# Kernel tuning notes

Hardware: AMD Instinct MI355X
Metric: run time of the kernel (lower is better)

The kernel has to match this reference:

```python
import jax, jax.numpy as jnp
import numpy as np

L = 4          # decoder layers (model_config "[4,[0],0]")
D = 1024       # d_model
H = 16         # n_head
DH = 64        # d_head
DI = 4096      # d_inner
V = 16000      # n_token (add_eot=False)
S = 1024       # seq len
B = 4          # batch
EPS = 1e-5


def _layer_norm(x, g, b):
    mu = jnp.mean(x, axis=-1, keepdims=True)
    var = jnp.mean(jnp.square(x - mu), axis=-1, keepdims=True)
    return (x - mu) * jax.lax.rsqrt(var + EPS) * g + b


def _rel_shift(x):
    # x: [b, n, q, k]
    b, n, q, k = x.shape
    zero_pad = jnp.zeros((b, n, q, 1), dtype=x.dtype)
    xp = jnp.concatenate([zero_pad, x], axis=3)        # [b,n,q,k+1]
    xp = xp.reshape(b, n, k + 1, q)
    return xp[:, :, 1:, :].reshape(b, n, q, k)


def setup_inputs() -> dict:
    key = jax.random.key(0)
    ks = list(jax.random.split(key, 24))
    sd = 0.02
    inp = {}
    inp["tokens"] = jax.random.randint(ks[0], (S, B), 0, V)
    inp["word_emb"] = jax.random.normal(ks[1], (V, D), jnp.float32) * sd
    inp["r_w_bias"] = jax.random.normal(ks[2], (H, DH), jnp.float32) * sd
    inp["r_r_bias"] = jax.random.normal(ks[3], (H, DH), jnp.float32) * sd
    inp["qkv_w"] = jax.random.normal(ks[4], (L, D, 3 * H * DH), jnp.float32) * sd
    inp["qkv_b"] = jnp.zeros((L, 3 * H * DH), jnp.float32)
    inp["r_kw"] = jax.random.normal(ks[5], (L, D, H * DH), jnp.float32) * sd
    inp["r_kb"] = jnp.zeros((L, H * DH), jnp.float32)
    inp["o_w"] = jax.random.normal(ks[6], (L, H * DH, D), jnp.float32) * sd
    inp["o_b"] = jnp.zeros((L, D), jnp.float32)
    inp["ln1_g"] = jnp.ones((L, D), jnp.float32)
    inp["ln1_b"] = jnp.zeros((L, D), jnp.float32)
    inp["ff1_w"] = jax.random.normal(ks[7], (L, D, DI), jnp.float32) * sd
    inp["ff1_b"] = jnp.zeros((L, DI), jnp.float32)
    inp["ff2_w"] = jax.random.normal(ks[8], (L, DI, D), jnp.float32) * sd
    inp["ff2_b"] = jnp.zeros((L, D), jnp.float32)
    inp["ln2_g"] = jnp.ones((L, D), jnp.float32)
    inp["ln2_b"] = jnp.zeros((L, D), jnp.float32)
    inp["final_w"] = jax.random.normal(ks[9], (D, V), jnp.float32) * sd
    inp["final_b"] = jnp.zeros((V,), jnp.float32)
    return inp


def reference(tokens, word_emb, r_w_bias, r_r_bias, qkv_w, qkv_b, r_kw, r_kb,
              o_w, o_b, ln1_g, ln1_b, ff1_w, ff1_b, ff2_w, ff2_b,
              ln2_g, ln2_b, final_w, final_b):
    s, b = tokens.shape
    h = word_emb[tokens]                                 # [S,B,D]
    # sinusoidal relative positions, pos_seq = klen-1 ... 0
    pos_seq = jnp.arange(s - 1, -1, -1, dtype=h.dtype)
    inv_freq = 1.0 / (10000.0 ** (jnp.arange(0, D, 2, dtype=h.dtype) / D))
    sinu = pos_seq[:, None] * inv_freq[None, :]
    r = jnp.concatenate([jnp.sin(sinu), jnp.cos(sinu)], axis=-1)   # [S,D]
    # causal mask: True = masked (j > i)
    mask = jnp.triu(jnp.ones((s, s), dtype=bool), k=1)
    scale = 1.0 / (DH ** 0.5)
    neg_inf = jnp.asarray(-jnp.inf, dtype=h.dtype)

    for l in range(L):
        qkv = h @ qkv_w[l] + qkv_b[l]                    # [S,B,3*H*DH]
        q, k, v = jnp.split(qkv, 3, axis=-1)
        q = q.reshape(s, b, H, DH)
        k = k.reshape(s, b, H, DH)
        v = v.reshape(s, b, H, DH)
        rk = (r @ r_kw[l] + r_kb[l]).reshape(s, H, DH)   # [S,H,DH]
        AC = jnp.einsum('ibnd,jbnd->bnij', q + r_w_bias, k)
        BD = jnp.einsum('ibnd,jnd->bnij', q + r_r_bias, rk)
        BD = _rel_shift(BD)
        score = scale * (AC + BD)
        score = jnp.where(mask[None, None, :, :], neg_inf, score)
        prob = jax.nn.softmax(score, axis=-1)
        vec = jnp.einsum('bnij,jbnd->ibnd', prob, v).reshape(s, b, H * DH)
        attn_out = vec @ o_w[l] + o_b[l]
        h = _layer_norm(h + attn_out, ln1_g[l], ln1_b[l])
        ff = jax.nn.gelu(h @ ff1_w[l] + ff1_b[l], approximate=False) @ ff2_w[l] + ff2_b[l]
        h = _layer_norm(h + ff, ln2_g[l], ln2_b[l])

    logits = h @ final_w + final_b                       # [S,B,V]
    return logits
```

## Files before the change

kernel.cpp:

```cpp
#include <hip/hip_runtime.h>

#define S 1024
#define Bb 4
#define Hh 16
#define DHh 64
#define Dm 1024
#define DIi 4096
#define Vv 16000
#define Lll 4

typedef __attribute__((ext_vector_type(4))) float f32x4;
typedef __attribute__((ext_vector_type(8))) __bf16 bf16x8;
typedef __attribute__((ext_vector_type(8))) unsigned short u16x8;
typedef __attribute__((ext_vector_type(4))) unsigned short u16x4;

__device__ __forceinline__ unsigned short f2bf(float f) {
  unsigned int u = __float_as_uint(f);
  u += 0x7fffu + ((u >> 16) & 1u);
  return (unsigned short)(u >> 16);
}
__device__ __forceinline__ float bf2f(unsigned short u) {
  return __uint_as_float(((unsigned int)u) << 16);
}

__device__ __forceinline__ void gload_lds16(const void* g, void* l) {
  __builtin_amdgcn_global_load_lds((const __attribute__((address_space(1))) unsigned int*)g,
                                   (__attribute__((address_space(3))) unsigned int*)l, 16, 0, 0);
}

__device__ __forceinline__ f32x4 mfma_bf16(bf16x8 a, bf16x8 b, f32x4 c) {
  return __builtin_amdgcn_mfma_f32_16x16x32_bf16(a, b, c, 0, 0, 0);
}

__global__ __launch_bounds__(256) void embed_k(const int* __restrict__ tokens,
                                               const float* __restrict__ we,
                                               float* __restrict__ h,
                                               unsigned short* __restrict__ hb) {
  int row = blockIdx.x;
  int t = threadIdx.x;
  int tok = tokens[row];
  f32x4 v = *(const f32x4*)&we[(long)tok * Dm + t * 4];
  *(f32x4*)&h[(long)row * Dm + t * 4] = v;
  u16x4 r;
#pragma unroll
  for (int e = 0; e < 4; ++e) r[e] = f2bf(v[e]);
  *(u16x4*)&hb[(long)row * Dm + t * 4] = r;
}

__global__ __launch_bounds__(256) void posr_k(unsigned short* __restrict__ r) {
  int idx = blockIdx.x * 256 + threadIdx.x;
  int u = idx >> 10, d = idx & 1023;
  float pos = (float)(S - 1 - u);
  int j = d & 511;
  float invf = powf(10000.0f, -(float)j * (1.0f / 512.0f));
  float a = pos * invf;
  r[idx] = f2bf(d < 512 ? sinf(a) : cosf(a));
}

__global__ __launch_bounds__(256) void wcvt_t(const float* __restrict__ W,
                                              unsigned short* __restrict__ WT,
                                              int Kd, int Nd) {
  __shared__ unsigned short tile[32][40];
  int n0 = blockIdx.x * 32, k0 = blockIdx.y * 32;
  const bool inb = n0 < Nd;
  const float* Wb = W + (long)blockIdx.z * Kd * Nd;
  unsigned short* WTb = WT + (long)blockIdx.z * Kd * Nd;
  int t = threadIdx.x;
  int rr = t >> 3, c4 = (t & 7) * 4;
  f32x4 v = {0.f, 0.f, 0.f, 0.f};
  if (inb) v = *(const f32x4*)&Wb[(long)(k0 + rr) * Nd + n0 + c4];
#pragma unroll
  for (int e = 0; e < 4; ++e) tile[rr][c4 + e] = f2bf(v[e]);
  __syncthreads();
  if (t < 128) {
    int n = t >> 2, k8 = (t & 3) * 8;
    u16x8 pk;
#pragma unroll
    for (int e = 0; e < 8; ++e) pk[e] = tile[k8 + e][n];
    *(u16x8*)&WTb[(long)(n0 + n) * Kd + k0 + k8] = pk;
  }
}

template <int EPI>
__global__ __launch_bounds__(512, 2) void gemm256(const unsigned short* __restrict__ A,
                                                  const unsigned short* __restrict__ BT,
                                                  const float* __restrict__ bias,
                                                  void* __restrict__ Cout,
                                                  int M, int N, int K,
                                                  int ntm, int ntn, int morder) {
  __shared__ unsigned short lds[65536];
  unsigned short* Al = lds;
  unsigned short* Bl = lds + 32768;
  const int tid = threadIdx.x, lane = tid & 63, w = tid >> 6;
  const int la = lane & 15, hi = lane >> 4;
  const int nwg = gridDim.x;
  const int qq = nwg >> 3, rr = nwg & 7;
  const int xcd = blockIdx.x & 7, loc = blockIdx.x >> 3;
  const int wg = (xcd < rr ? xcd * (qq + 1) : rr * (qq + 1) + (xcd - rr) * qq) + loc;
  int bm, bn;
  if (morder) { bm = (wg % ntm) * 256; bn = (wg / ntm) * 256; }
  else        { bn = (wg % ntn) * 256; bm = (wg / ntn) * 256; }
  const int wr = w >> 2, wc = w & 3;
  f32x4 acc[8][4] = {};

  const unsigned short* ag = A + (long)(bm + w * 16 + la) * K + hi * 8;
  const unsigned short* bg = BT + (long)(bn + w * 16 + la) * K + hi * 8;
  unsigned short* Asg = Al + w * 512;
  unsigned short* Bsg = Bl + w * 512;
  const unsigned short* Ard = Al + wr * 4096 + lane * 8;
  const unsigned short* Brd = Bl + wc * 2048 + lane * 8;
  const int NT = K >> 5;

#define STAGE(t) { \
    long ko_ = (long)(t) * 32; int bo_ = ((t) & 3) * 8192; \
    gload_lds16(ag + ko_, Asg + bo_); \
    gload_lds16(ag + ko_ + (long)128 * K, Asg + bo_ + 4096); \
    gload_lds16(bg + ko_, Bsg + bo_); \
    gload_lds16(bg + ko_ + (long)128 * K, Bsg + bo_ + 4096); }

#define COMPUTE(t) { \
    const int bo_ = ((t) & 3) * 8192; \
    bf16x8 af[8], bq[4]; \
    _Pragma("unroll") \
    for (int m = 0; m < 8; ++m) af[m] = *(const bf16x8*)(Ard + bo_ + m * 512); \
    _Pragma("unroll") \
    for (int n = 0; n < 4; ++n) bq[n] = *(const bf16x8*)(Brd + bo_ + n * 512); \
    __builtin_amdgcn_s_setprio(1); \
    _Pragma("unroll") \
    for (int m = 0; m < 8; ++m) \
      _Pragma("unroll") \
      for (int n = 0; n < 4; ++n) acc[m][n] = mfma_bf16(af[m], bq[n], acc[m][n]); \
    __builtin_amdgcn_s_setprio(0); }

  STAGE(0); STAGE(1); STAGE(2);
  int t = 0;
  for (; t < NT - 3; ++t) {
    asm volatile("s_waitcnt vmcnt(8)" ::: "memory");
    __builtin_amdgcn_s_barrier();
    __builtin_amdgcn_sched_barrier(0);
    STAGE(t + 3);
    COMPUTE(t);
  }
  asm volatile("s_waitcnt vmcnt(8)" ::: "memory");
  __builtin_amdgcn_s_barrier();
  __builtin_amdgcn_sched_barrier(0);
  COMPUTE(t); ++t;
  asm volatile("s_waitcnt vmcnt(4)" ::: "memory");
  __builtin_amdgcn_s_barrier();
  __builtin_amdgcn_sched_barrier(0);
  COMPUTE(t); ++t;
  asm volatile("s_waitcnt vmcnt(0)" ::: "memory");
  __builtin_amdgcn_s_barrier();
  __builtin_amdgcn_sched_barrier(0);
  COMPUTE(t);
#undef STAGE
#undef COMPUTE

#pragma unroll
  for (int m = 0; m < 8; ++m) {
#pragma unroll
    for (int n = 0; n < 4; ++n) {
      int col = bn + wc * 64 + n * 16 + la;
      if (col < N) {
        float bv = bias[col];
        int row = bm + wr * 128 + m * 16 + hi * 4;
#pragma unroll
        for (int e = 0; e < 4; ++e) {
          float v = acc[m][n][e] + bv;
          if (EPI == 0) {
            ((float*)Cout)[(long)(row + e) * N + col] = v;
          } else if (EPI == 1) {
            ((unsigned short*)Cout)[(long)(row + e) * N + col] = f2bf(v);
          } else {
            float g = 0.5f * v * (1.0f + erff(v * 0.70710678118f));
            ((unsigned short*)Cout)[(long)(row + e) * N + col] = f2bf(g);
          }
        }
      }
    }
  }
}

template <int EPI>
__global__ __launch_bounds__(256) void gemm_bt(const unsigned short* __restrict__ A,
                                               const unsigned short* __restrict__ BT,
                                               const float* __restrict__ bias,
                                               void* __restrict__ Cout,
                                               int M, int N, int K, int ntn) {
  __shared__ unsigned short As[128 * 64];
  __shared__ unsigned short Bs[128 * 64];
  const int tid = threadIdx.x;
  const int lane = tid & 63;
  const int w = tid >> 6;
  const int nwg = gridDim.x;
  const int qq = nwg >> 3, rr = nwg & 7;
  const int xcd = blockIdx.x & 7, loc = blockIdx.x >> 3;
  const int wg = (xcd < rr ? xcd * (qq + 1) : rr * (qq + 1) + (xcd - rr) * qq) + loc;
  const int bn = (wg % ntn) * 128, bm = (wg / ntn) * 128;
  const int wr = (w >> 1) * 64, wc = (w & 1) * 64;
  const int la = lane & 15, hi = lane >> 4;
  f32x4 acc[4][4] = {};

  const int rrow = tid >> 3;
  const int rcol = ((tid & 7) ^ (rrow & 7)) * 8;
  const unsigned short* ag = A + (long)(bm + rrow) * K + rcol;
  const unsigned short* bg = BT + (long)(bn + rrow) * K + rcol;
  const int las = la & 7;
  const int ro0 = (hi ^ las) * 8;
  const int ro1 = ((hi + 4) ^ las) * 8;

  for (int k0 = 0; k0 < K; k0 += 64) {
    __syncthreads();
#pragma unroll
    for (int c = 0; c < 4; ++c) {
      gload_lds16(ag + (long)c * 32 * K + k0, &As[c * 2048 + w * 512]);
      gload_lds16(bg + (long)c * 32 * K + k0, &Bs[c * 2048 + w * 512]);
    }
    __syncthreads();
#pragma unroll
    for (int kk = 0; kk < 2; ++kk) {
      const int ro = kk ? ro1 : ro0;
      bf16x8 af[4], bq[4];
#pragma unroll
      for (int mi = 0; mi < 4; ++mi)
        af[mi] = *(const bf16x8*)&As[(wr + mi * 16 + la) * 64 + ro];
#pragma unroll
      for (int ni = 0; ni < 4; ++ni)
        bq[ni] = *(const bf16x8*)&Bs[(wc + ni * 16 + la) * 64 + ro];
#pragma unroll
      for (int mi = 0; mi < 4; ++mi)
#pragma unroll
        for (int ni = 0; ni < 4; ++ni)
          acc[mi][ni] = mfma_bf16(af[mi], bq[ni], acc[mi][ni]);
    }
  }
  const int cr = hi * 4;
#pragma unroll
  for (int mi = 0; mi < 4; ++mi) {
#pragma unroll
    for (int ni = 0; ni < 4; ++ni) {
      int col = bn + wc + ni * 16 + la;
      float bv = bias[col];
      int row = bm + wr + mi * 16 + cr;
#pragma unroll
      for (int e = 0; e < 4; ++e) {
        float v = acc[mi][ni][e] + bv;
        if (EPI == 0) {
          ((float*)Cout)[(long)(row + e) * N + col] = v;
        } else if (EPI == 1) {
          ((unsigned short*)Cout)[(long)(row + e) * N + col] = f2bf(v);
        } else {
          float g = 0.5f * v * (1.0f + erff(v * 0.70710678118f));
          ((unsigned short*)Cout)[(long)(row + e) * N + col] = f2bf(g);
        }
      }
    }
  }
}

template <int EPI>
__global__ __launch_bounds__(256) void gemm_bt64(const unsigned short* __restrict__ A,
                                                 const unsigned short* __restrict__ BT,
                                                 const float* __restrict__ bias,
                                                 void* __restrict__ Cout,
                                                 int M, int N, int K, int ntn) {
  __shared__ unsigned short As[64 * 64];
  __shared__ unsigned short Bs[128 * 64];
  const int tid = threadIdx.x;
  const int lane = tid & 63;
  const int w = tid >> 6;
  const int nwg = gridDim.x;
  const int qq = nwg >> 3, rr = nwg & 7;
  const int xcd = blockIdx.x & 7, loc = blockIdx.x >> 3;
  const int wg = (xcd < rr ? xcd * (qq + 1) : rr * (qq + 1) + (xcd - rr) * qq) + loc;
  const int bn = (wg % ntn) * 128, bm = (wg / ntn) * 64;
  const int wr = (w >> 1) * 32, wc = (w & 1) * 64;
  const int la = lane & 15, hi = lane >> 4;
  f32x4 acc[2][4] = {};

  const int rrow = tid >> 3;
  const int rcol = ((tid & 7) ^ (rrow & 7)) * 8;
  const unsigned short* ag = A + (long)(bm + rrow) * K + rcol;
  const unsigned short* bg = BT + (long)(bn + rrow) * K + rcol;
  const int las = la & 7;
  const int ro0 = (hi ^ las) * 8;
  const int ro1 = ((hi + 4) ^ las) * 8;

  for (int k0 = 0; k0 < K; k0 += 64) {
    __syncthreads();
#pragma unroll
    for (int c = 0; c < 2; ++c)
      gload_lds16(ag + (long)c * 32 * K + k0, &As[c * 2048 + w * 512]);
#pragma unroll
    for (int c = 0; c < 4; ++c)
      gload_lds16(bg + (long)c * 32 * K + k0, &Bs[c * 2048 + w * 512]);
    __syncthreads();
#pragma unroll
    for (int kk = 0; kk < 2; ++kk) {
      const int ro = kk ? ro1 : ro0;
      bf16x8 af[2], bq[4];
#pragma unroll
      for (int mi = 0; mi < 2; ++mi)
        af[mi] = *(const bf16x8*)&As[(wr + mi * 16 + la) * 64 + ro];
#pragma unroll
      for (int ni = 0; ni < 4; ++ni)
        bq[ni] = *(const bf16x8*)&Bs[(wc + ni * 16 + la) * 64 + ro];
#pragma unroll
      for (int mi = 0; mi < 2; ++mi)
#pragma unroll
        for (int ni = 0; ni < 4; ++ni)
          acc[mi][ni] = mfma_bf16(af[mi], bq[ni], acc[mi][ni]);
    }
  }
  const int cr = hi * 4;
#pragma unroll
  for (int mi = 0; mi < 2; ++mi) {
#pragma unroll
    for (int ni = 0; ni < 4; ++ni) {
      int col = bn + wc + ni * 16 + la;
      float bv = bias[col];
      int row = bm + wr + mi * 16 + cr;
#pragma unroll
      for (int e = 0; e < 4; ++e) {
        float v = acc[mi][ni][e] + bv;
        if (EPI == 0) {
          ((float*)Cout)[(long)(row + e) * N + col] = v;
        } else if (EPI == 1) {
          ((unsigned short*)Cout)[(long)(row + e) * N + col] = f2bf(v);
        } else {
          float g = 0.5f * v * (1.0f + erff(v * 0.70710678118f));
          ((unsigned short*)Cout)[(long)(row + e) * N + col] = f2bf(g);
        }
      }
    }
  }
}

__global__ __launch_bounds__(256) void qkv_prep(const unsigned short* __restrict__ q3,
                                                const float* __restrict__ rwb,
                                                const float* __restrict__ rrb,
                                                unsigned short* __restrict__ qw,
                                                unsigned short* __restrict__ qr,
                                                unsigned short* __restrict__ kb) {
  int idx = blockIdx.x * 256 + threadIdx.x;
  int c8 = (idx & 127) * 8;
  int row = idx >> 7;
  int s = row >> 2, b = row & 3;
  int n = c8 >> 6, d = c8 & 63;
  u16x8 qv = *(const u16x8*)&q3[(long)row * 3072 + c8];
  u16x8 kv = *(const u16x8*)&q3[(long)row * 3072 + 1024 + c8];
  long o = ((long)(b * Hh + n) * S + s) * 64 + d;
  u16x8 ow, orr;
#pragma unroll
  for (int e = 0; e < 8; ++e) {
    float q = bf2f(qv[e]);
    ow[e] = f2bf(q + rwb[c8 + e]);
    orr[e] = f2bf(q + rrb[c8 + e]);
  }
  *(u16x8*)&qw[o] = ow;
  *(u16x8*)&qr[o] = orr;
  *(u16x8*)&kb[o] = kv;
}

__global__ __launch_bounds__(256) void vt_prep(const unsigned short* __restrict__ q3,
                                               unsigned short* __restrict__ vT) {
  __shared__ unsigned short tile[64][72];
  const int it = blockIdx.x, bn = blockIdx.y;
  const int nh = bn & 15, bbv = bn >> 4;
  const int t = threadIdx.x;
  const int i0 = t >> 3, c8 = (t & 7) * 8;
#pragma unroll
  for (int c = 0; c < 2; ++c) {
    int i = i0 + c * 32;
    u16x8 v = *(const u16x8*)&q3[((long)(it * 64 + i) * Bb + bbv) * 3072 + 2048 + nh * 64 + c8];
    *(u16x8*)&tile[i][c8] = v;
  }
  __syncthreads();
  for (int cc = t; cc < 512; cc += 256) {
    int d = cc >> 3, i8 = (cc & 7) * 8;
    u16x8 pk;
#pragma unroll
    for (int e = 0; e < 8; ++e) pk[e] = tile[i8 + e][d];
    *(u16x8*)&vT[((long)bn * 64 + d) * S + it * 64 + i8] = pk;
  }
}

__global__ __launch_bounds__(256) void rkb_prep(const unsigned short* __restrict__ rkall,
                                                unsigned short* __restrict__ rkb) {
  int idx = blockIdx.x * 256 + threadIdx.x;
  int d8 = (idx & 7) * 8;
  int u = (idx >> 3) & 1023;
  int nl = idx >> 13;
  int l = nl >> 4, n = nl & 15;
  u16x8 v = *(const u16x8*)&rkall[(long)u * 4096 + l * 1024 + n * 64 + d8];
  *(u16x8*)&rkb[(long)idx * 8] = v;
}

__global__ __launch_bounds__(256) void attn_k(const unsigned short* __restrict__ qw,
                                              const unsigned short* __restrict__ qr,
                                              const unsigned short* __restrict__ kbuf,
                                              const unsigned short* __restrict__ vT,
                                              const unsigned short* __restrict__ rk,
                                              unsigned short* __restrict__ vec) {
  __shared__ unsigned short Ks[2][64 * 64];
  __shared__ unsigned short Vs[2][64 * 64];
  __shared__ unsigned short plds[4][16][72];
  const int tid = threadIdx.x, lane = tid & 63, w = tid >> 6;
  const int bn = blockIdx.x >> 3, pr = blockIdx.x & 7;
  const int nh = bn & 15, bbv = bn >> 4;
  const int la = lane & 15, hi = lane >> 4, lk = hi * 8;
  const int hi4 = hi * 4;
  const unsigned short* kbase = kbuf + (long)bn * S * 64;
  const unsigned short* vbase = vT + (long)bn * 64 * S;
  const unsigned short* rbase = rk + (long)nh * S * 64;

  const int q0 = w * 128 + lane;
  const int r0 = q0 >> 3, c0s = (q0 & 7) ^ (r0 & 7);
  const int q1 = q0 + 64;
  const int r1 = q1 >> 3, c1s = (q1 & 7) ^ (r1 & 7);

  int cur = 0;
#pragma unroll 1
  for (int half = 0; half < 2; ++half) {
    const int it = half ? (15 - pr) : pr;
    const int iw = it * 64 + w * 16;
    bf16x8 qwf[2], qrf[2];
    {
      const unsigned short* qp = qw + ((long)bn * S + iw + la) * 64 + lk;
      qwf[0] = *(const bf16x8*)qp;
      qwf[1] = *(const bf16x8*)(qp + 32);
      const unsigned short* qp2 = qr + ((long)bn * S + iw + la) * 64 + lk;
      qrf[0] = *(const bf16x8*)qp2;
      qrf[1] = *(const bf16x8*)(qp2 + 32);
    }
    f32x4 opv[4] = {};
    float m_ = -3e38f;
    float l_[4] = {0.f, 0.f, 0.f, 0.f};

    gload_lds16(kbase + (long)r0 * 64 + c0s * 8, &Ks[cur][w * 1024]);
    gload_lds16(kbase + (long)r1 * 64 + c1s * 8, &Ks[cur][w * 1024 + 512]);
    gload_lds16(vbase + (long)r0 * S + c0s * 8, &Vs[cur][w * 1024]);
    gload_lds16(vbase + (long)r1 * S + c1s * 8, &Vs[cur][w * 1024 + 512]);
    __syncthreads();

    for (int jt = 0; jt <= it; ++jt) {
      const int j0 = jt * 64;
      const bool edge = (jt == it);
      if (jt < it) {
        const int jn = j0 + 64;
        gload_lds16(kbase + (long)(jn + r0) * 64 + c0s * 8, &Ks[cur ^ 1][w * 1024]);
        gload_lds16(kbase + (long)(jn + r1) * 64 + c1s * 8, &Ks[cur ^ 1][w * 1024 + 512]);
        gload_lds16(vbase + (long)r0 * S + jn + c0s * 8, &Vs[cur ^ 1][w * 1024]);
        gload_lds16(vbase + (long)r1 * S + jn + c1s * 8, &Vs[cur ^ 1][w * 1024 + 512]);
      }
      const int u0 = S - 16 - iw + j0;
      bf16x8 rf[10];
#pragma unroll
      for (int g = 0; g < 5; ++g) {
        int u = u0 + g * 16 + la;
        if (edge) u = (u > S - 1) ? (S - 1) : u;
        const unsigned short* rp = rbase + (long)u * 64 + lk;
        rf[2 * g] = *(const bf16x8*)rp;
        rf[2 * g + 1] = *(const bf16x8*)(rp + 32);
      }
      f32x4 ac[4] = {};
#pragma unroll
      for (int f = 0; f < 4; ++f) {
        int row = f * 16 + la;
        const unsigned short* kl = &Ks[cur][row * 64];
        bf16x8 k0 = *(const bf16x8*)(kl + (((hi) ^ (row & 7)) << 3));
        bf16x8 k1 = *(const bf16x8*)(kl + (((hi + 4) ^ (row & 7)) << 3));
        ac[f] = mfma_bf16(qwf[0], k0, ac[f]);
        ac[f] = mfma_bf16(qwf[1], k1, ac[f]);
      }
      f32x4 gg[5] = {};
#pragma unroll
      for (int g = 0; g < 5; ++g) {
        gg[g] = mfma_bf16(qrf[0], rf[2 * g], gg[g]);
        gg[g] = mfma_bf16(qrf[1], rf[2 * g + 1], gg[g]);
      }
      float p[4][4];
#pragma unroll
      for (int f = 0; f < 4; ++f) {
#pragma unroll
        for (int e = 0; e < 4; ++e) {
          int r = hi4 + e;
          float x = (la >= 15 - r) ? gg[f][e] : gg[f + 1][e];
          int src = (lane & 48) | ((la + 15 - r) & 15);
          float bd = __shfl(x, src, 64);
          float sc = (ac[f][e] + bd) * 0.125f;
          if (edge) {
            int i_ = iw + r, j_ = j0 + f * 16 + la;
            sc = (j_ > i_) ? -1e30f : sc;
          }
          p[f][e] = sc;
        }
      }
      float mx = p[0][0];
#pragma unroll
      for (int f = 0; f < 4; ++f)
#pragma unroll
        for (int e = 0; e < 4; ++e) mx = fmaxf(mx, p[f][e]);
#pragma unroll
      for (int o = 1; o < 16; o <<= 1) mx = fmaxf(mx, __shfl_xor(mx, o, 64));
      if (!__all(mx <= m_ + 8.0f)) {
        float mnew = fmaxf(m_, mx);
        float alpha = __expf(m_ - mnew);
        m_ = mnew;
#pragma unroll
        for (int e = 0; e < 4; ++e) l_[e] *= alpha;
#pragma unroll
        for (int d = 0; d < 4; ++d)
#pragma unroll
          for (int e = 0; e < 4; ++e) opv[d][e] *= alpha;
      }
#pragma unroll
      for (int e = 0; e < 4; ++e) {
        float rs = 0.f;
#pragma unroll
        for (int f = 0; f < 4; ++f) {
          p[f][e] = __expf(p[f][e] - m_);
          rs += p[f][e];
        }
        l_[e] += rs;
      }
#pragma unroll
      for (int f = 0; f < 4; ++f)
#pragma unroll
        for (int e = 0; e < 4; ++e)
          plds[w][hi4 + e][f * 16 + la] = f2bf(p[f][e]);
      bf16x8 pa0 = *(const bf16x8*)&plds[w][la][lk];
      bf16x8 pa1 = *(const bf16x8*)&plds[w][la][32 + lk];
#pragma unroll
      for (int d = 0; d < 4; ++d) {
        int dd = d * 16 + la;
        const unsigned short* vl = &Vs[cur][dd * 64];
        bf16x8 v0 = *(const bf16x8*)(vl + (((hi) ^ (dd & 7)) << 3));
        bf16x8 v1 = *(const bf16x8*)(vl + (((hi + 4) ^ (dd & 7)) << 3));
        opv[d] = mfma_bf16(pa0, v0, opv[d]);
        opv[d] = mfma_bf16(pa1, v1, opv[d]);
      }
      __syncthreads();
      if (jt < it) cur ^= 1;
    }
#pragma unroll
    for (int e = 0; e < 4; ++e) {
#pragma unroll
      for (int o = 1; o < 16; o <<= 1) l_[e] += __shfl_xor(l_[e], o, 64);
    }
#pragma unroll
    for (int d = 0; d < 4; ++d) {
#pragma unroll
      for (int e = 0; e < 4; ++e) {
        int i_ = iw + hi4 + e;
        int col = nh * 64 + d * 16 + la;
        vec[((long)i_ * Bb + bbv) * 1024 + col] = f2bf(opv[d][e] / l_[e]);
      }
    }
  }
}

__global__ __launch_bounds__(256) void add_ln(float* __restrict__ h, const float* __restrict__ x,
                                              const float* __restrict__ g, const float* __restrict__ b,
                                              unsigned short* __restrict__ hb) {
  __shared__ float red[8];
  int row = blockIdx.x, t = threadIdx.x;
  long base = (long)row * 1024 + t * 4;
  f32x4 hv = *(const f32x4*)&h[base];
  f32x4 xv = *(const f32x4*)&x[base];
  f32x4 y = hv + xv;
  float s = y[0] + y[1] + y[2] + y[3];
  float q = y[0] * y[0] + y[1] * y[1] + y[2] * y[2] + y[3] * y[3];
#pragma unroll
  for (int o = 1; o < 64; o <<= 1) {
    s += __shfl_xor(s, o, 64);
    q += __shfl_xor(q, o, 64);
  }
  int w = t >> 6, lane = t & 63;
  if (lane == 0) { red[w] = s; red[4 + w] = q; }
  __syncthreads();
  s = red[0] + red[1] + red[2] + red[3];
  q = red[4] + red[5] + red[6] + red[7];
  float mu = s * (1.0f / 1024.0f);
  float var = q * (1.0f / 1024.0f) - mu * mu;
  float rstd = rsqrtf(var + 1e-5f);
  f32x4 gv = *(const f32x4*)&g[t * 4];
  f32x4 bv = *(const f32x4*)&b[t * 4];
  f32x4 o;
  u16x4 ob;
#pragma unroll
  for (int e = 0; e < 4; ++e) {
    o[e] = (y[e] - mu) * rstd * gv[e] + bv[e];
    ob[e] = f2bf(o[e]);
  }
  *(f32x4*)&h[base] = o;
  *(u16x4*)&hb[base] = ob;
}

extern "C" void kernel_launch(void* const* d_in, const int* in_sizes, int n_in,
                              void* d_out, int out_size, void* d_ws, size_t ws_size,
                              hipStream_t stream) {
  const int* tokens = (const int*)d_in[0];
  const float* word_emb = (const float*)d_in[1];
  const float* rwb = (const float*)d_in[2];
  const float* rrb = (const float*)d_in[3];
  const float* qkv_w = (const float*)d_in[4];
  const float* qkv_b = (const float*)d_in[5];
  const float* r_kw = (const float*)d_in[6];
  const float* r_kb = (const float*)d_in[7];
  const float* o_w = (const float*)d_in[8];
  const float* o_b = (const float*)d_in[9];
  const float* ln1g = (const float*)d_in[10];
  const float* ln1b = (const float*)d_in[11];
  const float* ff1w = (const float*)d_in[12];
  const float* ff1b = (const float*)d_in[13];
  const float* ff2w = (const float*)d_in[14];
  const float* ff2b = (const float*)d_in[15];
  const float* ln2g = (const float*)d_in[16];
  const float* ln2b = (const float*)d_in[17];
  const float* fw = (const float*)d_in[18];
  const float* fb = (const float*)d_in[19];

  char* ws = (char*)d_ws;
  unsigned short* WBF = (unsigned short*)(ws);
  float* H = (float*)(ws + 33554432);
  unsigned short* HB = (unsigned short*)(ws + 50331648);
  unsigned short* GB = (unsigned short*)(ws + 58720256);
  unsigned short* RBF = (unsigned short*)(ws + 92274688);

  char* ob = (char*)d_out;
  float* OUTF = (float*)ob;
  unsigned short* OUTH = (unsigned short*)ob;
  unsigned short* QW = (unsigned short*)(ob + 67108864);
  unsigned short* QR = (unsigned short*)(ob + 75497472);
  unsigned short* KB = (unsigned short*)(ob + 83886080);
  unsigned short* VT = (unsigned short*)(ob + 92274688);
  unsigned short* RKB = (unsigned short*)(ob + 100663296);
  float* OUT = (float*)d_out;

  embed_k<<<4096, 256, 0, stream>>>(tokens, word_emb, H, HB);
  posr_k<<<4096, 256, 0, stream>>>(RBF);
  wcvt_t<<<dim3(32, 32, 4), 256, 0, stream>>>(r_kw, WBF, 1024, 1024);
  gemm_bt<1><<<256, 256, 0, stream>>>(RBF, WBF, r_kb, OUTH, 1024, 4096, 1024, 32);
  rkb_prep<<<2048, 256, 0, stream>>>(OUTH, RKB);

  for (int l = 0; l < Lll; ++l) {
    wcvt_t<<<dim3(96, 32, 1), 256, 0, stream>>>(qkv_w + (long)l * 1024 * 3072, WBF, 1024, 3072);
    gemm_bt<1><<<768, 256, 0, stream>>>(HB, WBF, qkv_b + l * 3072, OUTH, 4096, 3072, 1024, 24);
    qkv_prep<<<2048, 256, 0, stream>>>(OUTH, rwb, rrb, QW, QR, KB);
    vt_prep<<<dim3(16, 64), 256, 0, stream>>>(OUTH, VT);
    attn_k<<<512, 256, 0, stream>>>(QW, QR, KB, VT, RKB + (long)l * Hh * S * 64, HB);
    wcvt_t<<<dim3(32, 32, 1), 256, 0, stream>>>(o_w + (long)l * 1024 * 1024, WBF, 1024, 1024);
    gemm_bt64<0><<<512, 256, 0, stream>>>(HB, WBF, o_b + l * 1024, OUTF, 4096, 1024, 1024, 8);
    add_ln<<<4096, 256, 0, stream>>>(H, OUTF, ln1g + l * 1024, ln1b + l * 1024, HB);

    wcvt_t<<<dim3(128, 32, 1), 256, 0, stream>>>(ff1w + (long)l * 1024 * 4096, WBF, 1024, 4096);
    gemm_bt<2><<<1024, 256, 0, stream>>>(HB, WBF, ff1b + l * 4096, GB, 4096, 4096, 1024, 32);
    wcvt_t<<<dim3(32, 128, 1), 256, 0, stream>>>(ff2w + (long)l * 4096 * 1024, WBF, 4096, 1024);
    gemm_bt64<0><<<512, 256, 0, stream>>>(GB, WBF, ff2b + l * 1024, OUTF, 4096, 1024, 4096, 8);
    add_ln<<<4096, 256, 0, stream>>>(H, OUTF, ln2g + l * 1024, ln2b + l * 1024, HB);
  }

  wcvt_t<<<dim3(504, 32, 1), 256, 0, stream>>>(fw, WBF, 1024, 16000);
  gemm256<0><<<1008, 512, 0, stream>>>(HB, WBF, fb, OUT, 4096, 16000, 1024, 16, 63, 1);
}
```

Measured before the change: 1.418 ms.

## Fuse QKV head-layout prep into GEMM epilogue and split attention blocks per tile

The QKV GEMM gets a new epilogue that adds the relative biases and scatters Q and K directly into head-major buffers, and writes V into a compact buffer. This removes the separate qkv_prep kernel and its full read and write of the QKV output. The attention kernel now runs one query tile per block over a doubled grid, ordered from the largest causal tiles down, instead of pairing short and long tiles in one block. The cost is scattered 2-byte stores in the GEMM epilogue and more reliance on the hardware scheduler to balance attention work.

```diff
diff --git a/kernel.cpp b/kernel.cpp
--- a/kernel.cpp
+++ b/kernel.cpp
@@ -186,7 +186,13 @@
                                                const unsigned short* __restrict__ BT,
                                                const float* __restrict__ bias,
                                                void* __restrict__ Cout,
-                                               int M, int N, int K, int ntn) {
+                                               int M, int N, int K, int ntn,
+                                               const float* __restrict__ rwb,
+                                               const float* __restrict__ rrb,
+                                               unsigned short* __restrict__ qw,
+                                               unsigned short* __restrict__ qr,
+                                               unsigned short* __restrict__ kb,
+                                               unsigned short* __restrict__ vout) {
   __shared__ unsigned short As[128 * 64];
   __shared__ unsigned short Bs[128 * 64];
   const int tid = threadIdx.x;
@@ -242,16 +248,39 @@
       int col = bn + wc + ni * 16 + la;
       float bv = bias[col];
       int row = bm + wr + mi * 16 + cr;
-#pragma unroll
-      for (int e = 0; e < 4; ++e) {
-        float v = acc[mi][ni][e] + bv;
-        if (EPI == 0) {
-          ((float*)Cout)[(long)(row + e) * N + col] = v;
-        } else if (EPI == 1) {
-          ((unsigned short*)Cout)[(long)(row + e) * N + col] = f2bf(v);
-        } else {
-          float g = 0.5f * v * (1.0f + erff(v * 0.70710678118f));
-          ((unsigned short*)Cout)[(long)(row + e) * N + col] = f2bf(g);
+      if (EPI == 3) {
+        int t3 = col >> 10;
+        int c1 = col & 1023;
+        int n = c1 >> 6, d = c1 & 63;
+        float rw = (t3 == 0) ? rwb[c1] : 0.f;
+        float rrv = (t3 == 0) ? rrb[c1] : 0.f;
+#pragma unroll
+        for (int e = 0; e < 4; ++e) {
+          float v = acc[mi][ni][e] + bv;
+          int rowe = row + e;
+          int s = rowe >> 2, b = rowe & 3;
+          long o = ((long)(b * Hh + n) * S + s) * 64 + d;
+          if (t3 == 0) {
+            qw[o] = f2bf(v + rw);
+            qr[o] = f2bf(v + rrv);
+          } else if (t3 == 1) {
+            kb[o] = f2bf(v);
+          } else {
+            vout[(long)rowe * 1024 + c1] = f2bf(v);
+          }
+        }
+      } else {
+#pragma unroll
+        for (int e = 0; e < 4; ++e) {
+          float v = acc[mi][ni][e] + bv;
+          if (EPI == 0) {
+            ((float*)Cout)[(long)(row + e) * N + col] = v;
+          } else if (EPI == 1) {
+            ((unsigned short*)Cout)[(long)(row + e) * N + col] = f2bf(v);
+          } else {
+            float g = 0.5f * v * (1.0f + erff(v * 0.70710678118f));
+            ((unsigned short*)Cout)[(long)(row + e) * N + col] = f2bf(g);
+          }
         }
       }
     }
@@ -336,33 +365,7 @@
   }
 }
 
-__global__ __launch_bounds__(256) void qkv_prep(const unsigned short* __restrict__ q3,
-                                                const float* __restrict__ rwb,
-                                                const float* __restrict__ rrb,
-                                                unsigned short* __restrict__ qw,
-                                                unsigned short* __restrict__ qr,
-                                                unsigned short* __restrict__ kb) {
-  int idx = blockIdx.x * 256 + threadIdx.x;
-  int c8 = (idx & 127) * 8;
-  int row = idx >> 7;
-  int s = row >> 2, b = row & 3;
-  int n = c8 >> 6, d = c8 & 63;
-  u16x8 qv = *(const u16x8*)&q3[(long)row * 3072 + c8];
-  u16x8 kv = *(const u16x8*)&q3[(long)row * 3072 + 1024 + c8];
-  long o = ((long)(b * Hh + n) * S + s) * 64 + d;
-  u16x8 ow, orr;
-#pragma unroll
-  for (int e = 0; e < 8; ++e) {
-    float q = bf2f(qv[e]);
-    ow[e] = f2bf(q + rwb[c8 + e]);
-    orr[e] = f2bf(q + rrb[c8 + e]);
-  }
-  *(u16x8*)&qw[o] = ow;
-  *(u16x8*)&qr[o] = orr;
-  *(u16x8*)&kb[o] = kv;
-}
-
-__global__ __launch_bounds__(256) void vt_prep(const unsigned short* __restrict__ q3,
+__global__ __launch_bounds__(256) void vt_prep(const unsigned short* __restrict__ vin,
                                                unsigned short* __restrict__ vT) {
   __shared__ unsigned short tile[64][72];
   const int it = blockIdx.x, bn = blockIdx.y;
@@ -372,7 +375,7 @@
 #pragma unroll
   for (int c = 0; c < 2; ++c) {
     int i = i0 + c * 32;
-    u16x8 v = *(const u16x8*)&q3[((long)(it * 64 + i) * Bb + bbv) * 3072 + 2048 + nh * 64 + c8];
+    u16x8 v = *(const u16x8*)&vin[((long)(it * 64 + i) * Bb + bbv) * 1024 + nh * 64 + c8];
     *(u16x8*)&tile[i][c8] = v;
   }
   __syncthreads();
@@ -406,7 +409,8 @@
   __shared__ unsigned short Vs[2][64 * 64];
   __shared__ unsigned short plds[4][16][72];
   const int tid = threadIdx.x, lane = tid & 63, w = tid >> 6;
-  const int bn = blockIdx.x >> 3, pr = blockIdx.x & 7;
+  const int bn = blockIdx.x & 63;
+  const int it = 15 - (blockIdx.x >> 6);
   const int nh = bn & 15, bbv = bn >> 4;
   const int la = lane & 15, hi = lane >> 4, lk = hi * 8;
   const int hi4 = hi * 4;
@@ -419,143 +423,139 @@
   const int q1 = q0 + 64;
   const int r1 = q1 >> 3, c1s = (q1 & 7) ^ (r1 & 7);
 
+  const int iw = it * 64 + w * 16;
+  bf16x8 qwf[2], qrf[2];
+  {
+    const unsigned short* qp = qw + ((long)bn * S + iw + la) * 64 + lk;
+    qwf[0] = *(const bf16x8*)qp;
+    qwf[1] = *(const bf16x8*)(qp + 32);
+    const unsigned short* qp2 = qr + ((long)bn * S + iw + la) * 64 + lk;
+    qrf[0] = *(const bf16x8*)qp2;
+    qrf[1] = *(const bf16x8*)(qp2 + 32);
+  }
+  f32x4 opv[4] = {};
+  float m_ = -3e38f;
+  float l_[4] = {0.f, 0.f, 0.f, 0.f};
   int cur = 0;
-#pragma unroll 1
-  for (int half = 0; half < 2; ++half) {
-    const int it = half ? (15 - pr) : pr;
-    const int iw = it * 64 + w * 16;
-    bf16x8 qwf[2], qrf[2];
-    {
-      const unsigned short* qp = qw + ((long)bn * S + iw + la) * 64 + lk;
-      qwf[0] = *(const bf16x8*)qp;
-      qwf[1] = *(const bf16x8*)(qp + 32);
-      const unsigned short* qp2 = qr + ((long)bn * S + iw + la) * 64 + lk;
-      qrf[0] = *(const bf16x8*)qp2;
-      qrf[1] = *(const bf16x8*)(qp2 + 32);
-    }
-    f32x4 opv[4] = {};
-    float m_ = -3e38f;
-    float l_[4] = {0.f, 0.f, 0.f, 0.f};
-
-    gload_lds16(kbase + (long)r0 * 64 + c0s * 8, &Ks[cur][w * 1024]);
-    gload_lds16(kbase + (long)r1 * 64 + c1s * 8, &Ks[cur][w * 1024 + 512]);
-    gload_lds16(vbase + (long)r0 * S + c0s * 8, &Vs[cur][w * 1024]);
-    gload_lds16(vbase + (long)r1 * S + c1s * 8, &Vs[cur][w * 1024 + 512]);
+
+  gload_lds16(kbase + (long)r0 * 64 + c0s * 8, &Ks[cur][w * 1024]);
+  gload_lds16(kbase + (long)r1 * 64 + c1s * 8, &Ks[cur][w * 1024 + 512]);
+  gload_lds16(vbase + (long)r0 * S + c0s * 8, &Vs[cur][w * 1024]);
+  gload_lds16(vbase + (long)r1 * S + c1s * 8, &Vs[cur][w * 1024 + 512]);
+  __syncthreads();
+
+  for (int jt = 0; jt <= it; ++jt) {
+    const int j0 = jt * 64;
+    const bool edge = (jt == it);
+    if (jt < it) {
+      const int jn = j0 + 64;
+      gload_lds16(kbase + (long)(jn + r0) * 64 + c0s * 8, &Ks[cur ^ 1][w * 1024]);
+      gload_lds16(kbase + (long)(jn + r1) * 64 + c1s * 8, &Ks[cur ^ 1][w * 1024 + 512]);
+      gload_lds16(vbase + (long)r0 * S + jn + c0s * 8, &Vs[cur ^ 1][w * 1024]);
+      gload_lds16(vbase + (long)r1 * S + jn + c1s * 8, &Vs[cur ^ 1][w * 1024 + 512]);
+    }
+    const int u0 = S - 16 - iw + j0;
+    bf16x8 rf[10];
+#pragma unroll
+    for (int g = 0; g < 5; ++g) {
+      int u = u0 + g * 16 + la;
+      if (edge) u = (u > S - 1) ? (S - 1) : u;
+      const unsigned short* rp = rbase + (long)u * 64 + lk;
+      rf[2 * g] = *(const bf16x8*)rp;
+      rf[2 * g + 1] = *(const bf16x8*)(rp + 32);
+    }
+    f32x4 ac[4] = {};
+#pragma unroll
+    for (int f = 0; f < 4; ++f) {
+      int row = f * 16 + la;
+      const unsigned short* kl = &Ks[cur][row * 64];
+      bf16x8 k0 = *(const bf16x8*)(kl + (((hi) ^ (row & 7)) << 3));
+      bf16x8 k1 = *(const bf16x8*)(kl + (((hi + 4) ^ (row & 7)) << 3));
+      ac[f] = mfma_bf16(qwf[0], k0, ac[f]);
+      ac[f] = mfma_bf16(qwf[1], k1, ac[f]);
+    }
+    f32x4 gg[5] = {};
+#pragma unroll
+    for (int g = 0; g < 5; ++g) {
+      gg[g] = mfma_bf16(qrf[0], rf[2 * g], gg[g]);
+      gg[g] = mfma_bf16(qrf[1], rf[2 * g + 1], gg[g]);
+    }
+    float p[4][4];
+#pragma unroll
+    for (int f = 0; f < 4; ++f) {
+#pragma unroll
+      for (int e = 0; e < 4; ++e) {
+        int r = hi4 + e;
+        float x = (la >= 15 - r) ? gg[f][e] : gg[f + 1][e];
+        int src = (lane & 48) | ((la + 15 - r) & 15);
+        float bd = __shfl(x, src, 64);
+        float sc = (ac[f][e] + bd) * 0.125f;
+        if (edge) {
+          int i_ = iw + r, j_ = j0 + f * 16 + la;
+          sc = (j_ > i_) ? -1e30f : sc;
+        }
+        p[f][e] = sc;
+      }
+    }
+    float mx = p[0][0];
+#pragma unroll
+    for (int f = 0; f < 4; ++f)
+#pragma unroll
+      for (int e = 0; e < 4; ++e) mx = fmaxf(mx, p[f][e]);
+#pragma unroll
+    for (int o = 1; o < 16; o <<= 1) mx = fmaxf(mx, __shfl_xor(mx, o, 64));
+    if (!__all(mx <= m_ + 8.0f)) {
+      float mnew = fmaxf(m_, mx);
+      float alpha = __expf(m_ - mnew);
+      m_ = mnew;
+#pragma unroll
+      for (int e = 0; e < 4; ++e) l_[e] *= alpha;
+#pragma unroll
+      for (int d = 0; d < 4; ++d)
+#pragma unroll
+        for (int e = 0; e < 4; ++e) opv[d][e] *= alpha;
+    }
+#pragma unroll
+    for (int e = 0; e < 4; ++e) {
+      float rs = 0.f;
+#pragma unroll
+      for (int f = 0; f < 4; ++f) {
+        p[f][e] = __expf(p[f][e] - m_);
+        rs += p[f][e];
+      }
+      l_[e] += rs;
+    }
+#pragma unroll
+    for (int f = 0; f < 4; ++f)
+#pragma unroll
+      for (int e = 0; e < 4; ++e)
+        plds[w][hi4 + e][f * 16 + la] = f2bf(p[f][e]);
+    bf16x8 pa0 = *(const bf16x8*)&plds[w][la][lk];
+    bf16x8 pa1 = *(const bf16x8*)&plds[w][la][32 + lk];
+#pragma unroll
+    for (int d = 0; d < 4; ++d) {
+      int dd = d * 16 + la;
+      const unsigned short* vl = &Vs[cur][dd * 64];
+      bf16x8 v0 = *(const bf16x8*)(vl + (((hi) ^ (dd & 7)) << 3));
+      bf16x8 v1 = *(const bf16x8*)(vl + (((hi + 4) ^ (dd & 7)) << 3));
+      opv[d] = mfma_bf16(pa0, v0, opv[d]);
+      opv[d] = mfma_bf16(pa1, v1, opv[d]);
+    }
     __syncthreads();
-
-    for (int jt = 0; jt <= it; ++jt) {
-      const int j0 = jt * 64;
-      const bool edge = (jt == it);
-      if (jt < it) {
-        const int jn = j0 + 64;
-        gload_lds16(kbase + (long)(jn + r0) * 64 + c0s * 8, &Ks[cur ^ 1][w * 1024]);
-        gload_lds16(kbase + (long)(jn + r1) * 64 + c1s * 8, &Ks[cur ^ 1][w * 1024 + 512]);
-        gload_lds16(vbase + (long)r0 * S + jn + c0s * 8, &Vs[cur ^ 1][w * 1024]);
-        gload_lds16(vbase + (long)r1 * S + jn + c1s * 8, &Vs[cur ^ 1][w * 1024 + 512]);
-      }
-      const int u0 = S - 16 - iw + j0;
-      bf16x8 rf[10];
-#pragma unroll
-      for (int g = 0; g < 5; ++g) {
-        int u = u0 + g * 16 + la;
-        if (edge) u = (u > S - 1) ? (S - 1) : u;
-        const unsigned short* rp = rbase + (long)u * 64 + lk;
-        rf[2 * g] = *(const bf16x8*)rp;
-        rf[2 * g + 1] = *(const bf16x8*)(rp + 32);
-      }
-      f32x4 ac[4] = {};
-#pragma unroll
-      for (int f = 0; f < 4; ++f) {
-        int row = f * 16 + la;
-        const unsigned short* kl = &Ks[cur][row * 64];
-        bf16x8 k0 = *(const bf16x8*)(kl + (((hi) ^ (row & 7)) << 3));
-        bf16x8 k1 = *(const bf16x8*)(kl + (((hi + 4) ^ (row & 7)) << 3));
-        ac[f] = mfma_bf16(qwf[0], k0, ac[f]);
-        ac[f] = mfma_bf16(qwf[1], k1, ac[f]);
-      }
-      f32x4 gg[5] = {};
-#pragma unroll
-      for (int g = 0; g < 5; ++g) {
-        gg[g] = mfma_bf16(qrf[0], rf[2 * g], gg[g]);
-        gg[g] = mfma_bf16(qrf[1], rf[2 * g + 1], gg[g]);
-      }
-      float p[4][4];
-#pragma unroll
-      for (int f = 0; f < 4; ++f) {
-#pragma unroll
-        for (int e = 0; e < 4; ++e) {
-          int r = hi4 + e;
-          float x = (la >= 15 - r) ? gg[f][e] : gg[f + 1][e];
-          int src = (lane & 48) | ((la + 15 - r) & 15);
-          float bd = __shfl(x, src, 64);
-          float sc = (ac[f][e] + bd) * 0.125f;
-          if (edge) {
-            int i_ = iw + r, j_ = j0 + f * 16 + la;
-            sc = (j_ > i_) ? -1e30f : sc;
-          }
-          p[f][e] = sc;
-        }
-      }
-      float mx = p[0][0];
-#pragma unroll
-      for (int f = 0; f < 4; ++f)
-#pragma unroll
-        for (int e = 0; e < 4; ++e) mx = fmaxf(mx, p[f][e]);
-#pragma unroll
-      for (int o = 1; o < 16; o <<= 1) mx = fmaxf(mx, __shfl_xor(mx, o, 64));
-      if (!__all(mx <= m_ + 8.0f)) {
-        float mnew = fmaxf(m_, mx);
-        float alpha = __expf(m_ - mnew);
-        m_ = mnew;
-#pragma unroll
-        for (int e = 0; e < 4; ++e) l_[e] *= alpha;
-#pragma unroll
-        for (int d = 0; d < 4; ++d)
-#pragma unroll
-          for (int e = 0; e < 4; ++e) opv[d][e] *= alpha;
-      }
-#pragma unroll
-      for (int e = 0; e < 4; ++e) {
-        float rs = 0.f;
-#pragma unroll
-        for (int f = 0; f < 4; ++f) {
-          p[f][e] = __expf(p[f][e] - m_);
-          rs += p[f][e];
-        }
-        l_[e] += rs;
-      }
-#pragma unroll
-      for (int f = 0; f < 4; ++f)
-#pragma unroll
-        for (int e = 0; e < 4; ++e)
-          plds[w][hi4 + e][f * 16 + la] = f2bf(p[f][e]);
-      bf16x8 pa0 = *(const bf16x8*)&plds[w][la][lk];
-      bf16x8 pa1 = *(const bf16x8*)&plds[w][la][32 + lk];
-#pragma unroll
-      for (int d = 0; d < 4; ++d) {
-        int dd = d * 16 + la;
-        const unsigned short* vl = &Vs[cur][dd * 64];
-        bf16x8 v0 = *(const bf16x8*)(vl + (((hi) ^ (dd & 7)) << 3));
-        bf16x8 v1 = *(const bf16x8*)(vl + (((hi + 4) ^ (dd & 7)) << 3));
-        opv[d] = mfma_bf16(pa0, v0, opv[d]);
-        opv[d] = mfma_bf16(pa1, v1, opv[d]);
-      }
-      __syncthreads();
-      if (jt < it) cur ^= 1;
-    }
+    if (jt < it) cur ^= 1;
+  }
+#pragma unroll
+  for (int e = 0; e < 4; ++e) {
+#pragma unroll
+    for (int o = 1; o < 16; o <<= 1) l_[e] += __shfl_xor(l_[e], o, 64);
+  }
+#pragma unroll
+  for (int d = 0; d < 4; ++d) {
 #pragma unroll
     for (int e = 0; e < 4; ++e) {
-#pragma unroll
-      for (int o = 1; o < 16; o <<= 1) l_[e] += __shfl_xor(l_[e], o, 64);
-    }
-#pragma unroll
-    for (int d = 0; d < 4; ++d) {
-#pragma unroll
-      for (int e = 0; e < 4; ++e) {
-        int i_ = iw + hi4 + e;
-        int col = nh * 64 + d * 16 + la;
-        vec[((long)i_ * Bb + bbv) * 1024 + col] = f2bf(opv[d][e] / l_[e]);
-      }
+      int i_ = iw + hi4 + e;
+      int col = nh * 64 + d * 16 + la;
+      vec[((long)i_ * Bb + bbv) * 1024 + col] = f2bf(opv[d][e] / l_[e]);
     }
   }
 }
@@ -641,21 +641,23 @@
   embed_k<<<4096, 256, 0, stream>>>(tokens, word_emb, H, HB);
   posr_k<<<4096, 256, 0, stream>>>(RBF);
   wcvt_t<<<dim3(32, 32, 4), 256, 0, stream>>>(r_kw, WBF, 1024, 1024);
-  gemm_bt<1><<<256, 256, 0, stream>>>(RBF, WBF, r_kb, OUTH, 1024, 4096, 1024, 32);
+  gemm_bt<1><<<256, 256, 0, stream>>>(RBF, WBF, r_kb, OUTH, 1024, 4096, 1024, 32,
+                                      nullptr, nullptr, nullptr, nullptr, nullptr, nullptr);
   rkb_prep<<<2048, 256, 0, stream>>>(OUTH, RKB);
 
   for (int l = 0; l < Lll; ++l) {
     wcvt_t<<<dim3(96, 32, 1), 256, 0, stream>>>(qkv_w + (long)l * 1024 * 3072, WBF, 1024, 3072);
-    gemm_bt<1><<<768, 256, 0, stream>>>(HB, WBF, qkv_b + l * 3072, OUTH, 4096, 3072, 1024, 24);
-    qkv_prep<<<2048, 256, 0, stream>>>(OUTH, rwb, rrb, QW, QR, KB);
+    gemm_bt<3><<<768, 256, 0, stream>>>(HB, WBF, qkv_b + l * 3072, nullptr, 4096, 3072, 1024, 24,
+                                        rwb, rrb, QW, QR, KB, OUTH);
     vt_prep<<<dim3(16, 64), 256, 0, stream>>>(OUTH, VT);
-    attn_k<<<512, 256, 0, stream>>>(QW, QR, KB, VT, RKB + (long)l * Hh * S * 64, HB);
+    attn_k<<<1024, 256, 0, stream>>>(QW, QR, KB, VT, RKB + (long)l * Hh * S * 64, HB);
     wcvt_t<<<dim3(32, 32, 1), 256, 0, stream>>>(o_w + (long)l * 1024 * 1024, WBF, 1024, 1024);
     gemm_bt64<0><<<512, 256, 0, stream>>>(HB, WBF, o_b + l * 1024, OUTF, 4096, 1024, 1024, 8);
     add_ln<<<4096, 256, 0, stream>>>(H, OUTF, ln1g + l * 1024, ln1b + l * 1024, HB);
 
     wcvt_t<<<dim3(128, 32, 1), 256, 0, stream>>>(ff1w + (long)l * 1024 * 4096, WBF, 1024, 4096);
-    gemm_bt<2><<<1024, 256, 0, stream>>>(HB, WBF, ff1b + l * 4096, GB, 4096, 4096, 1024, 32);
+    gemm_bt<2><<<1024, 256, 0, stream>>>(HB, WBF, ff1b + l * 4096, GB, 4096, 4096, 1024, 32,
+                                         nullptr, nullptr, nullptr, nullptr, nullptr, nullptr);
     wcvt_t<<<dim3(32, 128, 1), 256, 0, stream>>>(ff2w + (long)l * 4096 * 1024, WBF, 4096, 1024);
     gemm_bt64<0><<<512, 256, 0, stream>>>(GB, WBF, ff2b + l * 1024, OUTF, 4096, 1024, 4096, 8);
     add_ln<<<4096, 256, 0, stream>>>(H, OUTF, ln2g + l * 1024, ln2b + l * 1024, HB);
```

Result: slower. 1.556 ms (+9.8%).
